# Optimization experiments

Measured on AMD Instinct MI355X. Metric: run time of the kernel, lower is better.

The kernel has to match this reference:

```python
import jax, jax.numpy as jnp
import numpy as np
import math

H_DIM = 1024
N_HEADS = 16
B, T = 2, 2048


def setup_inputs() -> dict:
    key = jax.random.key(0)
    ks = jax.random.split(key, 9)
    scale = 1.0 / math.sqrt(H_DIM)
    x = jax.random.normal(ks[0], (B, T, H_DIM), dtype=jnp.float32)
    Wq = jax.random.normal(ks[1], (H_DIM, H_DIM), dtype=jnp.float32) * scale
    Wk = jax.random.normal(ks[2], (H_DIM, H_DIM), dtype=jnp.float32) * scale
    Wv = jax.random.normal(ks[3], (H_DIM, H_DIM), dtype=jnp.float32) * scale
    Wp = jax.random.normal(ks[4], (H_DIM, H_DIM), dtype=jnp.float32) * scale
    bq = jnp.zeros((H_DIM,), dtype=jnp.float32)
    bk = jnp.zeros((H_DIM,), dtype=jnp.float32)
    bv = jnp.zeros((H_DIM,), dtype=jnp.float32)
    bp = jnp.zeros((H_DIM,), dtype=jnp.float32)
    return {"x": x, "Wq": Wq, "bq": bq, "Wk": Wk, "bk": bk,
            "Wv": Wv, "bv": bv, "Wp": Wp, "bp": bp}


def _attention(x, Wq, bq, Wk, bk, Wv, bv, Wp, bp):
    Bx, Tx, C = x.shape
    N = N_HEADS
    D = C // N
    # torch Linear: x @ W.T + b
    q = (x @ Wq.T + bq).reshape(Bx, Tx, N, D).transpose(0, 2, 1, 3)  # [B,N,T,D]
    k = (x @ Wk.T + bk).reshape(Bx, Tx, N, D).transpose(0, 2, 1, 3)
    v = (x @ Wv.T + bv).reshape(Bx, Tx, N, D).transpose(0, 2, 1, 3)
    scores = jnp.einsum('bntd,bnsd->bnts', q, k) / math.sqrt(D)  # [B,N,T,T]
    causal = jnp.tril(jnp.ones((Tx, Tx), dtype=bool))
    scores = jnp.where(causal[None, None], scores, -jnp.inf)
    probs = jax.nn.softmax(scores, axis=-1)
    attn = jnp.einsum('bnts,bnsd->bntd', probs, v)  # [B,N,T,D]
    attn = attn.transpose(0, 2, 1, 3).reshape(Bx, Tx, C)
    return attn @ Wp.T + bp


def reference(x, Wq, bq, Wk, bk, Wv, bv, Wp, bp):
    return _attention(x, Wq, bq, Wk, bk, Wv, bv, Wp, bp)
```

## Files before the change

### kernel.cpp

```cpp
#include <hip/hip_runtime.h>
#include <hip/hip_bf16.h>
#include <math.h>

#define TSEQ 2048
#define CDIM 1024
#define NHEADS 16
#define DHEAD 64
#define BSZ 2
#define MROWS (BSZ * TSEQ)

typedef __attribute__((ext_vector_type(8))) short short8;
typedef __attribute__((ext_vector_type(4))) short short4v;
typedef __attribute__((ext_vector_type(4))) float f32x4;

__device__ inline f32x4 mfma16(short8 a, short8 b, f32x4 c) {
    return __builtin_amdgcn_mfma_f32_16x16x32_bf16(a, b, c, 0, 0, 0);
}

__device__ inline short f2bf(float f) {
    __hip_bfloat16 h = __float2bfloat16(f);
    return __builtin_bit_cast(short, h);
}
__device__ inline float bf2f(short s) {
    __hip_bfloat16 h = __builtin_bit_cast(__hip_bfloat16, s);
    return __bfloat162float(h);
}

__global__ __launch_bounds__(256) void convx_kernel(const float* __restrict__ x,
                                                    short* __restrict__ xb) {
    size_t off = (size_t)(blockIdx.x * 256 + threadIdx.x) * 8;
    float4 a = *(const float4*)(x + off);
    float4 b = *(const float4*)(x + off + 4);
    short8 h;
    h[0] = f2bf(a.x); h[1] = f2bf(a.y); h[2] = f2bf(a.z); h[3] = f2bf(a.w);
    h[4] = f2bf(b.x); h[5] = f2bf(b.y); h[6] = f2bf(b.z); h[7] = f2bf(b.w);
    *(short8*)(xb + off) = h;
}

__global__ __launch_bounds__(256) void gemm_qkv(
    const short* __restrict__ xb, const float* __restrict__ Wq,
    const float* __restrict__ Wk, const float* __restrict__ Wv,
    const float* __restrict__ bq, const float* __restrict__ bk,
    const float* __restrict__ bv, short* __restrict__ qws,
    short* __restrict__ kws, short* __restrict__ vtws) {
    __shared__ __attribute__((aligned(16))) short a_lds[128][40];
    __shared__ __attribute__((aligned(16))) short b_lds[128][40];

    const int tid = threadIdx.x;
    const int lane = tid & 63;
    const int wv = tid >> 6;
    const int wr = wv >> 1, wc = wv & 1;
    const int l15 = lane & 15, l4 = lane >> 4;
    const int mbase = blockIdx.x * 128;
    const int which = blockIdx.y >> 3;
    const int nbase = (blockIdx.y & 7) * 128;
    const float* Wf = which == 0 ? Wq : (which == 1 ? Wk : Wv);
    const float* bias = which == 0 ? bq : (which == 1 ? bk : bv);

    f32x4 acc[4][4];
#pragma unroll
    for (int i = 0; i < 4; ++i)
#pragma unroll
        for (int j = 0; j < 4; ++j) acc[i][j] = f32x4{0.f, 0.f, 0.f, 0.f};

    const int arow = tid >> 2;
    const int acol = (tid & 3) * 8;
    const int brow = tid >> 3;
    const int bcol = (tid & 7) * 4;
    const short* aptr = xb + (size_t)(mbase + arow) * CDIM + acol;
    const float* bptr = Wf + (size_t)(nbase + brow) * CDIM + bcol;

    short8 apre[2];
    float4 bpre[4];
    apre[0] = *(const short8*)(aptr);
    apre[1] = *(const short8*)(aptr + (size_t)64 * CDIM);
#pragma unroll
    for (int it = 0; it < 4; ++it)
        bpre[it] = *(const float4*)(bptr + (size_t)(it * 32) * CDIM);

    for (int k0 = 0; k0 < CDIM; k0 += 32) {
        __syncthreads();
        *(short8*)&a_lds[arow][acol] = apre[0];
        *(short8*)&a_lds[arow + 64][acol] = apre[1];
#pragma unroll
        for (int it = 0; it < 4; ++it) {
            short4v h;
            h.x = f2bf(bpre[it].x); h.y = f2bf(bpre[it].y);
            h.z = f2bf(bpre[it].z); h.w = f2bf(bpre[it].w);
            *(short4v*)&b_lds[brow + it * 32][bcol] = h;
        }
        __syncthreads();
        if (k0 + 32 < CDIM) {
            apre[0] = *(const short8*)(aptr + k0 + 32);
            apre[1] = *(const short8*)(aptr + (size_t)64 * CDIM + k0 + 32);
#pragma unroll
            for (int it = 0; it < 4; ++it)
                bpre[it] = *(const float4*)(bptr + (size_t)(it * 32) * CDIM + k0 + 32);
        }

        short8 af[4], bfr[4];
#pragma unroll
        for (int i = 0; i < 4; ++i)
            af[i] = *(const short8*)&a_lds[wr * 64 + i * 16 + l15][l4 * 8];
#pragma unroll
        for (int j = 0; j < 4; ++j)
            bfr[j] = *(const short8*)&b_lds[wc * 64 + j * 16 + l15][l4 * 8];
#pragma unroll
        for (int i = 0; i < 4; ++i)
#pragma unroll
            for (int j = 0; j < 4; ++j)
                acc[i][j] = mfma16(af[i], bfr[j], acc[i][j]);
    }

    if (which < 2) {
        short* dst = which == 0 ? qws : kws;
#pragma unroll
        for (int i = 0; i < 4; ++i) {
            int mrow = mbase + wr * 64 + i * 16 + l4 * 4;
#pragma unroll
            for (int j = 0; j < 4; ++j) {
                int o = nbase + wc * 64 + j * 16 + l15;
                int n = o >> 6, d = o & 63;
                float bval = bias[o];
#pragma unroll
                for (int r = 0; r < 4; ++r) {
                    int mm = mrow + r;
                    int bb = mm >> 11;
                    int t = mm & (TSEQ - 1);
                    dst[(((size_t)bb * NHEADS + n) * TSEQ + t) * DHEAD + d] =
                        f2bf(acc[i][j][r] + bval);
                }
            }
        }
    } else {
#pragma unroll
        for (int i = 0; i < 4; ++i) {
            int mrow = mbase + wr * 64 + i * 16 + l4 * 4;
            int bb = mrow >> 11;
            int t = mrow & (TSEQ - 1);
#pragma unroll
            for (int j = 0; j < 4; ++j) {
                int o = nbase + wc * 64 + j * 16 + l15;
                int n = o >> 6, d = o & 63;
                float bval = bias[o];
                short4v h4;
#pragma unroll
                for (int r = 0; r < 4; ++r) h4[r] = f2bf(acc[i][j][r] + bval);
                *(short4v*)&vtws[(((size_t)bb * NHEADS + n) * DHEAD + d) * TSEQ + t] = h4;
            }
        }
    }
}

__global__ __launch_bounds__(256) void gemm_p(
    const short* __restrict__ attn, const float* __restrict__ Wp,
    const float* __restrict__ bp, float* __restrict__ out) {
    __shared__ __attribute__((aligned(16))) short a_lds[64][40];
    __shared__ __attribute__((aligned(16))) short b_lds[128][40];

    const int tid = threadIdx.x;
    const int lane = tid & 63;
    const int wv = tid >> 6;
    const int wr = wv >> 1, wc = wv & 1;
    const int l15 = lane & 15, l4 = lane >> 4;
    const int mbase = blockIdx.x * 64;
    const int nbase = blockIdx.y * 128;

    f32x4 acc[2][4];
#pragma unroll
    for (int i = 0; i < 2; ++i)
#pragma unroll
        for (int j = 0; j < 4; ++j) acc[i][j] = f32x4{0.f, 0.f, 0.f, 0.f};

    const int arow = tid >> 2;
    const int acol = (tid & 3) * 8;
    const int brow = tid >> 3;
    const int bcol = (tid & 7) * 4;
    const short* aptr = attn + (size_t)(mbase + arow) * CDIM + acol;
    const float* bptr = Wp + (size_t)(nbase + brow) * CDIM + bcol;

    short8 apre;
    float4 bpre[4];
    apre = *(const short8*)(aptr);
#pragma unroll
    for (int it = 0; it < 4; ++it)
        bpre[it] = *(const float4*)(bptr + (size_t)(it * 32) * CDIM);

    for (int k0 = 0; k0 < CDIM; k0 += 32) {
        __syncthreads();
        *(short8*)&a_lds[arow][acol] = apre;
#pragma unroll
        for (int it = 0; it < 4; ++it) {
            short4v h;
            h.x = f2bf(bpre[it].x); h.y = f2bf(bpre[it].y);
            h.z = f2bf(bpre[it].z); h.w = f2bf(bpre[it].w);
            *(short4v*)&b_lds[brow + it * 32][bcol] = h;
        }
        __syncthreads();
        if (k0 + 32 < CDIM) {
            apre = *(const short8*)(aptr + k0 + 32);
#pragma unroll
            for (int it = 0; it < 4; ++it)
                bpre[it] = *(const float4*)(bptr + (size_t)(it * 32) * CDIM + k0 + 32);
        }

        short8 af[2], bfr[4];
#pragma unroll
        for (int i = 0; i < 2; ++i)
            af[i] = *(const short8*)&a_lds[wr * 32 + i * 16 + l15][l4 * 8];
#pragma unroll
        for (int j = 0; j < 4; ++j)
            bfr[j] = *(const short8*)&b_lds[wc * 64 + j * 16 + l15][l4 * 8];
#pragma unroll
        for (int i = 0; i < 2; ++i)
#pragma unroll
            for (int j = 0; j < 4; ++j)
                acc[i][j] = mfma16(af[i], bfr[j], acc[i][j]);
    }

#pragma unroll
    for (int i = 0; i < 2; ++i) {
        int mrow = mbase + wr * 32 + i * 16 + l4 * 4;
#pragma unroll
        for (int j = 0; j < 4; ++j) {
            int o = nbase + wc * 64 + j * 16 + l15;
            float bval = bp[o];
#pragma unroll
            for (int r = 0; r < 4; ++r)
                out[(size_t)(mrow + r) * CDIM + o] = acc[i][j][r] + bval;
        }
    }
}

__global__ __launch_bounds__(256) void attn_kernel(
    const short* __restrict__ q, const short* __restrict__ k,
    const short* __restrict__ vt, short* __restrict__ attn_out) {
    __shared__ __attribute__((aligned(16))) short k_lds[64][64];
    __shared__ __attribute__((aligned(16))) short vt_lds[64][64];
    __shared__ __attribute__((aligned(16))) short p_lds[4][16][80];

    const int tid = threadIdx.x;
    const int w = tid >> 6;
    const int lane = tid & 63;
    const int l15 = lane & 15;
    const int l4 = lane >> 4;
    const int h = blockIdx.x;
    const int qtile = gridDim.y - 1 - blockIdx.y;
    const int qb = qtile * 64;
    const int wrow0 = qb + w * 16;

    short8 qf[2];
#pragma unroll
    for (int kh = 0; kh < 2; ++kh) {
        const short* qp = q + ((size_t)h * TSEQ + wrow0 + l15) * DHEAD + kh * 32 + l4 * 8;
        short8 t8 = *(const short8*)qp;
#pragma unroll
        for (int e = 0; e < 8; ++e) t8[e] = f2bf(bf2f(t8[e]) * 0.125f);
        qf[kh] = t8;
    }

    float l_run[4];
    f32x4 o_acc[4];
#pragma unroll
    for (int r = 0; r < 4; ++r) l_run[r] = 0.f;
#pragma unroll
    for (int dt = 0; dt < 4; ++dt) o_acc[dt] = f32x4{0.f, 0.f, 0.f, 0.f};

    const int ntiles = qtile + 1;
    const int srow = tid >> 3;
    const int sgrp = tid & 7;

    short8 kpre[2], vpre[2];
#pragma unroll
    for (int it = 0; it < 2; ++it) {
        int row = srow + it * 32;
        kpre[it] = *(const short8*)(k + ((size_t)h * TSEQ + row) * DHEAD + sgrp * 8);
        vpre[it] = *(const short8*)(vt + ((size_t)h * DHEAD + row) * TSEQ + sgrp * 8);
    }

    for (int kvt = 0; kvt < ntiles; ++kvt) {
        const int kvbase = kvt * 64;
        __syncthreads();
#pragma unroll
        for (int it = 0; it < 2; ++it) {
            int row = srow + it * 32;
            int gs = sgrp ^ (row & 7);
            *(short8*)&k_lds[row][gs * 8] = kpre[it];
            *(short8*)&vt_lds[row][gs * 8] = vpre[it];
        }
        __syncthreads();
        if (kvt + 1 < ntiles) {
            int kvb2 = kvbase + 64;
#pragma unroll
            for (int it = 0; it < 2; ++it) {
                int row = srow + it * 32;
                kpre[it] = *(const short8*)(k + ((size_t)h * TSEQ + kvb2 + row) * DHEAD + sgrp * 8);
                vpre[it] = *(const short8*)(vt + ((size_t)h * DHEAD + row) * TSEQ + kvb2 + sgrp * 8);
            }
        }

        f32x4 s[4];
#pragma unroll
        for (int jt = 0; jt < 4; ++jt) {
            int row = jt * 16 + l15;
            int sw = row & 7;
            short8 kf0 = *(const short8*)&k_lds[row][(l4 ^ sw) * 8];
            short8 kf1 = *(const short8*)&k_lds[row][((4 + l4) ^ sw) * 8];
            f32x4 a = f32x4{0.f, 0.f, 0.f, 0.f};
            a = mfma16(qf[0], kf0, a);
            a = mfma16(qf[1], kf1, a);
            s[jt] = a;
        }

        const bool needmask = (kvbase + 63 > wrow0);
#pragma unroll
        for (int r = 0; r < 4; ++r) {
            int qrow = wrow0 + l4 * 4 + r;
            float lp = 0.f;
#pragma unroll
            for (int jt = 0; jt < 4; ++jt) {
                float x = s[jt][r];
                if (needmask && (kvbase + jt * 16 + l15 > qrow)) x = -INFINITY;
                float e = __expf(fminf(x, 60.f));
                lp += e;
                p_lds[w][l4 * 4 + r][jt * 16 + l15] = f2bf(e);
            }
            l_run[r] += lp;
        }

        short8 pa0 = *(const short8*)&p_lds[w][l15][l4 * 8];
        short8 pa1 = *(const short8*)&p_lds[w][l15][32 + l4 * 8];
#pragma unroll
        for (int dt = 0; dt < 4; ++dt) {
            int row = dt * 16 + l15;
            int sw = row & 7;
            short8 vf0 = *(const short8*)&vt_lds[row][(l4 ^ sw) * 8];
            short8 vf1 = *(const short8*)&vt_lds[row][((4 + l4) ^ sw) * 8];
            o_acc[dt] = mfma16(pa0, vf0, o_acc[dt]);
            o_acc[dt] = mfma16(pa1, vf1, o_acc[dt]);
        }
    }

#pragma unroll
    for (int r = 0; r < 4; ++r) {
        float l = l_run[r];
#pragma unroll
        for (int mk = 1; mk < 16; mk <<= 1) l += __shfl_xor(l, mk);
        l_run[r] = 1.0f / l;
    }
    const int b = h >> 4, n = h & 15;
#pragma unroll
    for (int dt = 0; dt < 4; ++dt) {
#pragma unroll
        for (int r = 0; r < 4; ++r) {
            int t = wrow0 + l4 * 4 + r;
            attn_out[((size_t)b * TSEQ + t) * CDIM + n * DHEAD + dt * 16 + l15] =
                f2bf(o_acc[dt][r] * l_run[r]);
        }
    }
}

extern "C" void kernel_launch(void* const* d_in, const int* in_sizes, int n_in,
                              void* d_out, int out_size, void* d_ws, size_t ws_size,
                              hipStream_t stream) {
    const float* x  = (const float*)d_in[0];
    const float* Wq = (const float*)d_in[1];
    const float* bq = (const float*)d_in[2];
    const float* Wk = (const float*)d_in[3];
    const float* bk = (const float*)d_in[4];
    const float* Wv = (const float*)d_in[5];
    const float* bv = (const float*)d_in[6];
    const float* Wp = (const float*)d_in[7];
    const float* bp = (const float*)d_in[8];

    char* ws = (char*)d_ws;
    const size_t SZ = (size_t)MROWS * CDIM * sizeof(short);
    short* qws  = (short*)(ws);
    short* kws  = (short*)(ws + SZ);
    short* vtws = (short*)(ws + 2 * SZ);
    short* xb   = (short*)(ws + 3 * SZ);
    short* attn = xb;

    convx_kernel<<<2048, 256, 0, stream>>>(x, xb);
    gemm_qkv<<<dim3(MROWS / 128, 24), 256, 0, stream>>>(xb, Wq, Wk, Wv, bq, bk, bv,
                                                         qws, kws, vtws);
    attn_kernel<<<dim3(BSZ * NHEADS, TSEQ / 64), 256, 0, stream>>>(qws, kws, vtws, attn);
    gemm_p<<<dim3(MROWS / 64, CDIM / 128), 256, 0, stream>>>(attn, Wp, bp, (float*)d_out);
}
```

Measured before the change: 114.0 us.

## Deepen QKV GEMM K-step and load attention K/V fragments directly from global

The QKV projection GEMM now stages 64-wide K slices per iteration with larger LDS tiles and an occupancy hint, halving the barriers per output tile. The attention kernel no longer stages K and V^T tiles in shared memory; each wave reads its MFMA fragments straight from global memory. This removes two block-wide barriers per KV tile and the LDS staging. In exchange, each wave fetches the same K/V data redundantly and loses the register prefetch, so it relies on cache hits to hide latency.

```diff
diff --git a/kernel.cpp b/kernel.cpp
--- a/kernel.cpp
+++ b/kernel.cpp
@@ -37,14 +37,14 @@
     *(short8*)(xb + off) = h;
 }
 
-__global__ __launch_bounds__(256) void gemm_qkv(
+__global__ __launch_bounds__(256, 3) void gemm_qkv(
     const short* __restrict__ xb, const float* __restrict__ Wq,
     const float* __restrict__ Wk, const float* __restrict__ Wv,
     const float* __restrict__ bq, const float* __restrict__ bk,
     const float* __restrict__ bv, short* __restrict__ qws,
     short* __restrict__ kws, short* __restrict__ vtws) {
-    __shared__ __attribute__((aligned(16))) short a_lds[128][40];
-    __shared__ __attribute__((aligned(16))) short b_lds[128][40];
+    __shared__ __attribute__((aligned(16))) short a_lds[128][72];
+    __shared__ __attribute__((aligned(16))) short b_lds[128][72];
 
     const int tid = threadIdx.x;
     const int lane = tid & 63;
@@ -63,53 +63,59 @@
 #pragma unroll
         for (int j = 0; j < 4; ++j) acc[i][j] = f32x4{0.f, 0.f, 0.f, 0.f};
 
-    const int arow = tid >> 2;
-    const int acol = (tid & 3) * 8;
-    const int brow = tid >> 3;
-    const int bcol = (tid & 7) * 4;
-    const short* aptr = xb + (size_t)(mbase + arow) * CDIM + acol;
-    const float* bptr = Wf + (size_t)(nbase + brow) * CDIM + bcol;
-
-    short8 apre[2];
-    float4 bpre[4];
-    apre[0] = *(const short8*)(aptr);
-    apre[1] = *(const short8*)(aptr + (size_t)64 * CDIM);
+    const int ar = tid >> 3;
+    const int ag = (tid & 7) * 8;
+    const int br = tid >> 4;
+    const int bg = (tid & 15) * 4;
+    const short* aptr = xb + (size_t)(mbase + ar) * CDIM + ag;
+    const float* bptr = Wf + (size_t)(nbase + br) * CDIM + bg;
+
+    short8 apre[4];
+    float4 bpre[8];
 #pragma unroll
     for (int it = 0; it < 4; ++it)
-        bpre[it] = *(const float4*)(bptr + (size_t)(it * 32) * CDIM);
-
-    for (int k0 = 0; k0 < CDIM; k0 += 32) {
+        apre[it] = *(const short8*)(aptr + (size_t)(32 * it) * CDIM);
+#pragma unroll
+    for (int it = 0; it < 8; ++it)
+        bpre[it] = *(const float4*)(bptr + (size_t)(16 * it) * CDIM);
+
+    for (int k0 = 0; k0 < CDIM; k0 += 64) {
         __syncthreads();
-        *(short8*)&a_lds[arow][acol] = apre[0];
-        *(short8*)&a_lds[arow + 64][acol] = apre[1];
-#pragma unroll
-        for (int it = 0; it < 4; ++it) {
+#pragma unroll
+        for (int it = 0; it < 4; ++it)
+            *(short8*)&a_lds[ar + 32 * it][ag] = apre[it];
+#pragma unroll
+        for (int it = 0; it < 8; ++it) {
             short4v h;
             h.x = f2bf(bpre[it].x); h.y = f2bf(bpre[it].y);
             h.z = f2bf(bpre[it].z); h.w = f2bf(bpre[it].w);
-            *(short4v*)&b_lds[brow + it * 32][bcol] = h;
+            *(short4v*)&b_lds[br + 16 * it][bg] = h;
         }
         __syncthreads();
-        if (k0 + 32 < CDIM) {
-            apre[0] = *(const short8*)(aptr + k0 + 32);
-            apre[1] = *(const short8*)(aptr + (size_t)64 * CDIM + k0 + 32);
+        if (k0 + 64 < CDIM) {
 #pragma unroll
             for (int it = 0; it < 4; ++it)
-                bpre[it] = *(const float4*)(bptr + (size_t)(it * 32) * CDIM + k0 + 32);
-        }
-
-        short8 af[4], bfr[4];
-#pragma unroll
-        for (int i = 0; i < 4; ++i)
-            af[i] = *(const short8*)&a_lds[wr * 64 + i * 16 + l15][l4 * 8];
-#pragma unroll
-        for (int j = 0; j < 4; ++j)
-            bfr[j] = *(const short8*)&b_lds[wc * 64 + j * 16 + l15][l4 * 8];
-#pragma unroll
-        for (int i = 0; i < 4; ++i)
+                apre[it] = *(const short8*)(aptr + (size_t)(32 * it) * CDIM + k0 + 64);
+#pragma unroll
+            for (int it = 0; it < 8; ++it)
+                bpre[it] = *(const float4*)(bptr + (size_t)(16 * it) * CDIM + k0 + 64);
+        }
+
+#pragma unroll
+        for (int kk = 0; kk < 2; ++kk) {
+            short8 af[4], bfr[4];
+#pragma unroll
+            for (int i = 0; i < 4; ++i)
+                af[i] = *(const short8*)&a_lds[wr * 64 + i * 16 + l15][kk * 32 + l4 * 8];
 #pragma unroll
             for (int j = 0; j < 4; ++j)
-                acc[i][j] = mfma16(af[i], bfr[j], acc[i][j]);
+                bfr[j] = *(const short8*)&b_lds[wc * 64 + j * 16 + l15][kk * 32 + l4 * 8];
+#pragma unroll
+            for (int i = 0; i < 4; ++i)
+#pragma unroll
+                for (int j = 0; j < 4; ++j)
+                    acc[i][j] = mfma16(af[i], bfr[j], acc[i][j]);
+        }
     }
 
     if (which < 2) {
@@ -235,8 +241,6 @@
 __global__ __launch_bounds__(256) void attn_kernel(
     const short* __restrict__ q, const short* __restrict__ k,
     const short* __restrict__ vt, short* __restrict__ attn_out) {
-    __shared__ __attribute__((aligned(16))) short k_lds[64][64];
-    __shared__ __attribute__((aligned(16))) short vt_lds[64][64];
     __shared__ __attribute__((aligned(16))) short p_lds[4][16][80];
 
     const int tid = threadIdx.x;
@@ -246,8 +250,7 @@
     const int l4 = lane >> 4;
     const int h = blockIdx.x;
     const int qtile = gridDim.y - 1 - blockIdx.y;
-    const int qb = qtile * 64;
-    const int wrow0 = qb + w * 16;
+    const int wrow0 = qtile * 64 + w * 16;
 
     short8 qf[2];
 #pragma unroll
@@ -266,46 +269,19 @@
 #pragma unroll
     for (int dt = 0; dt < 4; ++dt) o_acc[dt] = f32x4{0.f, 0.f, 0.f, 0.f};
 
+    const short* kbase = k + (size_t)h * TSEQ * DHEAD;
+    const short* vbase = vt + (size_t)h * DHEAD * TSEQ;
     const int ntiles = qtile + 1;
-    const int srow = tid >> 3;
-    const int sgrp = tid & 7;
-
-    short8 kpre[2], vpre[2];
-#pragma unroll
-    for (int it = 0; it < 2; ++it) {
-        int row = srow + it * 32;
-        kpre[it] = *(const short8*)(k + ((size_t)h * TSEQ + row) * DHEAD + sgrp * 8);
-        vpre[it] = *(const short8*)(vt + ((size_t)h * DHEAD + row) * TSEQ + sgrp * 8);
-    }
 
     for (int kvt = 0; kvt < ntiles; ++kvt) {
         const int kvbase = kvt * 64;
-        __syncthreads();
-#pragma unroll
-        for (int it = 0; it < 2; ++it) {
-            int row = srow + it * 32;
-            int gs = sgrp ^ (row & 7);
-            *(short8*)&k_lds[row][gs * 8] = kpre[it];
-            *(short8*)&vt_lds[row][gs * 8] = vpre[it];
-        }
-        __syncthreads();
-        if (kvt + 1 < ntiles) {
-            int kvb2 = kvbase + 64;
-#pragma unroll
-            for (int it = 0; it < 2; ++it) {
-                int row = srow + it * 32;
-                kpre[it] = *(const short8*)(k + ((size_t)h * TSEQ + kvb2 + row) * DHEAD + sgrp * 8);
-                vpre[it] = *(const short8*)(vt + ((size_t)h * DHEAD + row) * TSEQ + kvb2 + sgrp * 8);
-            }
-        }
 
         f32x4 s[4];
 #pragma unroll
         for (int jt = 0; jt < 4; ++jt) {
-            int row = jt * 16 + l15;
-            int sw = row & 7;
-            short8 kf0 = *(const short8*)&k_lds[row][(l4 ^ sw) * 8];
-            short8 kf1 = *(const short8*)&k_lds[row][((4 + l4) ^ sw) * 8];
+            const short* kr = kbase + (size_t)(kvbase + jt * 16 + l15) * DHEAD;
+            short8 kf0 = *(const short8*)(kr + l4 * 8);
+            short8 kf1 = *(const short8*)(kr + 32 + l4 * 8);
             f32x4 a = f32x4{0.f, 0.f, 0.f, 0.f};
             a = mfma16(qf[0], kf0, a);
             a = mfma16(qf[1], kf1, a);
@@ -332,10 +308,9 @@
         short8 pa1 = *(const short8*)&p_lds[w][l15][32 + l4 * 8];
 #pragma unroll
         for (int dt = 0; dt < 4; ++dt) {
-            int row = dt * 16 + l15;
-            int sw = row & 7;
-            short8 vf0 = *(const short8*)&vt_lds[row][(l4 ^ sw) * 8];
-            short8 vf1 = *(const short8*)&vt_lds[row][((4 + l4) ^ sw) * 8];
+            const short* vr = vbase + (size_t)(dt * 16 + l15) * TSEQ + kvbase;
+            short8 vf0 = *(const short8*)(vr + l4 * 8);
+            short8 vf1 = *(const short8*)(vr + 32 + l4 * 8);
             o_acc[dt] = mfma16(pa0, vf0, o_acc[dt]);
             o_acc[dt] = mfma16(pa1, vf1, o_acc[dt]);
         }
```

Measured after the change: 212.3 us. 1.86x slower.
